# Kernel optimization log

Hardware: AMD Instinct MI355X
Metric: run time of the kernel (lower is better)

The kernel has to match this reference:

```python
import jax, jax.numpy as jnp
import numpy as np

B, S, H, D = 8, 4096, 16, 128

def setup_inputs() -> dict:
    key = jax.random.key(0)
    kq, kk, kv = jax.random.split(key, 3)
    q = jax.random.normal(kq, (B, S, H, D), dtype=jnp.float32)
    k = jax.random.normal(kk, (B, S, H, D), dtype=jnp.float32)
    v = jax.random.normal(kv, (B, S, H, D), dtype=jnp.float32)
    return {"q": q, "k": k, "v": v}

def reference(q, k, v):
    # Efficient (linear) attention: softmax K over sequence, softmax Q over feature dim,
    # then context = K^T V per (batch, head), out = Q @ context. Vectorized over heads.
    k_sm = jax.nn.softmax(k, axis=1)          # softmax over S  (B,S,H,D)
    q_sm = jax.nn.softmax(q, axis=-1)         # softmax over D  (B,S,H,D)
    context = jnp.einsum('bshd,bshe->bhde', k_sm, v)   # (B,H,Dk,Dv)
    out = jnp.einsum('bshd,bhde->bshe', q_sm, context) # (B,S,H,Dv)
    return out
```

## Files before the change

kernel.cpp:

```cpp
#include <hip/hip_runtime.h>

using bf16x8 = __attribute__((ext_vector_type(8))) short;
using f32x4  = __attribute__((ext_vector_type(4))) float;

static constexpr int NB = 8;
static constexpr int NS = 4096;
static constexpr int NH = 16;
static constexpr int ND = 128;
static constexpr int BH = NB * NH;
static constexpr int HD = NH * ND;

__device__ inline unsigned pack2(float a, float b) {
    unsigned ua = __float_as_uint(a), ub = __float_as_uint(b);
    ua += 0x7fffu + ((ua >> 16) & 1u);
    ub += 0x7fffu + ((ub >> 16) & 1u);
    return (ua >> 16) | (ub & 0xffff0000u);
}

__device__ inline int swzh(int row) { return (row ^ (row >> 2)) & 7; }

template <int NC>
__global__ __launch_bounds__(256, 2)
void ctx_mfma(const float* __restrict__ kk, const float* __restrict__ vv,
              float* __restrict__ pctx_t, float* __restrict__ pden) {
    constexpr int SC = NS / NC;
    constexpr int T  = SC / 64;
    __shared__ __align__(16) unsigned short aL[2][128][64];
    __shared__ __align__(16) unsigned short bL[2][128][64];

    const int blk = blockIdx.x, bh = blk / NC, c = blk % NC;
    const int b = bh >> 4, h = bh & 15;
    const int tid = threadIdx.x, lane = tid & 63, wv = tid >> 6;
    const int r15 = lane & 15, hi = lane >> 4;
    const size_t base = (size_t)b * NS * HD + (size_t)h * ND;

    const int d0 = (tid & 31) * 4;
    const int sg = tid >> 5;

    float dsum[4] = {0.f, 0.f, 0.f, 0.f};

    auto stage = [&](int t, int buf) {
        const size_t s0 = (size_t)(c * SC + t * 64 + 8 * sg);
        const float* kp = kk + base + s0 * HD + d0;
        const float* vp = vv + base + s0 * HD + d0;
        float4 kq[8], vq[8];
#pragma unroll
        for (int j = 0; j < 8; ++j) kq[j] = *(const float4*)(kp + (size_t)j * HD);
#pragma unroll
        for (int j = 0; j < 8; ++j) vq[j] = *(const float4*)(vp + (size_t)j * HD);
        float ek[8][4];
        const float* kf = (const float*)kq;
        const float* vf = (const float*)vq;
#pragma unroll
        for (int j = 0; j < 8; ++j)
#pragma unroll
            for (int i = 0; i < 4; ++i) {
                ek[j][i] = __expf(kf[4 * j + i]);
                dsum[i] += ek[j][i];
            }
#pragma unroll
        for (int i = 0; i < 4; ++i) {
            const int row = d0 + i;
            const int cw = sg ^ swzh(row);
            *(uint4*)&aL[buf][row][cw * 8] = make_uint4(
                pack2(ek[0][i], ek[1][i]), pack2(ek[2][i], ek[3][i]),
                pack2(ek[4][i], ek[5][i]), pack2(ek[6][i], ek[7][i]));
            *(uint4*)&bL[buf][row][cw * 8] = make_uint4(
                pack2(vf[0 + i], vf[4 + i]), pack2(vf[8 + i], vf[12 + i]),
                pack2(vf[16 + i], vf[20 + i]), pack2(vf[24 + i], vf[28 + i]));
        }
    };

    f32x4 acc[4][4];
#pragma unroll
    for (int m = 0; m < 4; ++m)
#pragma unroll
        for (int n = 0; n < 4; ++n) acc[m][n] = (f32x4){0.f, 0.f, 0.f, 0.f};

    const int wd = wv >> 1, we = wv & 1;

    stage(0, 0);
    for (int t = 0; t < T; ++t) {
        __syncthreads();
        if (t + 1 < T) stage(t + 1, (t + 1) & 1);
        const int buf = t & 1;
#pragma unroll
        for (int ks = 0; ks < 2; ++ks) {
            bf16x8 af[4], bfv[4];
#pragma unroll
            for (int m = 0; m < 4; ++m) {
                const int row = 64 * wd + 16 * m + r15;
                const int cw = (4 * ks + hi) ^ swzh(row);
                af[m] = *(const bf16x8*)&aL[buf][row][cw * 8];
            }
#pragma unroll
            for (int n = 0; n < 4; ++n) {
                const int row = 64 * we + 16 * n + r15;
                const int cw = (4 * ks + hi) ^ swzh(row);
                bfv[n] = *(const bf16x8*)&bL[buf][row][cw * 8];
            }
#pragma unroll
            for (int m = 0; m < 4; ++m)
#pragma unroll
                for (int n = 0; n < 4; ++n)
                    acc[m][n] = __builtin_amdgcn_mfma_f32_16x16x32_bf16(
                        af[m], bfv[n], acc[m][n], 0, 0, 0);
        }
    }

    __syncthreads();
    float* dr = (float*)&aL[0][0][0];
    *(float4*)&dr[sg * 128 + d0] = make_float4(dsum[0], dsum[1], dsum[2], dsum[3]);
    __syncthreads();
    if (tid < 128) {
        float s = 0.f;
#pragma unroll
        for (int r = 0; r < 8; ++r) s += dr[r * 128 + tid];
        pden[(size_t)blk * 128 + tid] = s;
    }

    float* po = pctx_t + (size_t)blk * (ND * ND);
#pragma unroll
    for (int m = 0; m < 4; ++m)
#pragma unroll
        for (int n = 0; n < 4; ++n) {
            const int e  = 64 * we + 16 * n + r15;
            const int dd = 64 * wd + 16 * m + 4 * hi;
            *(f32x4*)&po[e * ND + dd] = acc[m][n];
        }
}

__global__ void ctx_combine(const float* __restrict__ pctx_t,
                            const float* __restrict__ pden,
                            unsigned short* __restrict__ ctx_t, int nc) {
    const int gid = blockIdx.x * 256 + threadIdx.x;
    const size_t w = (size_t)gid * 2;
    const int bh = (int)(w >> 14);
    const int wi = (int)(w & 16383);
    const int dd = wi & 127;
    float s0 = 0.f, s1 = 0.f, dn0 = 0.f, dn1 = 0.f;
    for (int c2 = 0; c2 < nc; ++c2) {
        const float* p  = pctx_t + (((size_t)(bh * nc + c2)) << 14) + wi;
        const float* pd = pden + (size_t)(bh * nc + c2) * ND + dd;
        s0 += p[0]; s1 += p[1];
        dn0 += pd[0]; dn1 += pd[1];
    }
    *(unsigned*)&ctx_t[w] = pack2(s0 / dn0, s1 / dn1);
}

__global__ __launch_bounds__(256, 2)
void out_mfma(const float* __restrict__ qq,
              const unsigned short* __restrict__ ctx_t,
              float* __restrict__ out) {
    __shared__ __align__(16) unsigned short cL[128][128];
    __shared__ __align__(16) unsigned short qL[2][32][128];
    __shared__ float qd[2][32];

    const int blk = blockIdx.x, bh = blk >> 3, c = blk & 7;
    const int b = bh >> 4, h = bh & 15;
    const int tid = threadIdx.x, lane = tid & 63, wv = tid >> 6;
    const int r15 = lane & 15, hi = lane >> 4;

    {
        const unsigned short* src = ctx_t + ((size_t)bh << 14);
#pragma unroll
        for (int j = 0; j < 8; ++j) {
            const int g = tid + 256 * j;
            const int e = g >> 4, cs = g & 15;
            uint4 t4 = *(const uint4*)&src[e * 128 + cs * 8];
            *(uint4*)&cL[e][(cs ^ (e & 15)) * 8] = t4;
        }
    }

    const size_t qbase = (size_t)b * NS * HD + (size_t)h * ND;
    const int s_blk = c * 512;

    auto stageq = [&](int t, int buf) {
#pragma unroll
        for (int jj = 0; jj < 2; ++jj) {
            const int g = tid + 256 * jj;
            const int s = g >> 4, cs = g & 15;
            const float* qp = qq + qbase + (size_t)(s_blk + t * 32 + s) * HD + cs * 8;
            float x[8];
            *(float4*)&x[0] = *(const float4*)qp;
            *(float4*)&x[4] = *(const float4*)(qp + 4);
            float ps = 0.f;
            unsigned pw[4];
#pragma unroll
            for (int j2 = 0; j2 < 4; ++j2) {
                float e0 = __expf(x[2 * j2]), e1 = __expf(x[2 * j2 + 1]);
                ps += e0 + e1;
                pw[j2] = pack2(e0, e1);
            }
            ps += __shfl_xor(ps, 1);
            ps += __shfl_xor(ps, 2);
            ps += __shfl_xor(ps, 4);
            ps += __shfl_xor(ps, 8);
            *(uint4*)&qL[buf][s][(cs ^ (s & 15)) * 8] =
                make_uint4(pw[0], pw[1], pw[2], pw[3]);
            if ((lane & 15) == 0) qd[buf][s] = ps;
        }
    };

    __syncthreads();

    bf16x8 bfr[2][4];
#pragma unroll
    for (int n = 0; n < 2; ++n) {
        const int e = 32 * wv + 16 * n + r15;
#pragma unroll
        for (int ks = 0; ks < 4; ++ks) {
            const int cw = (4 * ks + hi) ^ (e & 15);
            bfr[n][ks] = *(const bf16x8*)&cL[e][cw * 8];
        }
    }

    stageq(0, 0);
    for (int t = 0; t < 16; ++t) {
        __syncthreads();
        if (t + 1 < 16) stageq(t + 1, (t + 1) & 1);
        const int buf = t & 1;

        f32x4 acc[2][2];
#pragma unroll
        for (int m = 0; m < 2; ++m)
#pragma unroll
            for (int n = 0; n < 2; ++n) acc[m][n] = (f32x4){0.f, 0.f, 0.f, 0.f};

#pragma unroll
        for (int ks = 0; ks < 4; ++ks) {
            bf16x8 af[2];
#pragma unroll
            for (int m = 0; m < 2; ++m) {
                const int s = 16 * m + r15;
                const int cw = (4 * ks + hi) ^ (s & 15);
                af[m] = *(const bf16x8*)&qL[buf][s][cw * 8];
            }
#pragma unroll
            for (int m = 0; m < 2; ++m)
#pragma unroll
                for (int n = 0; n < 2; ++n)
                    acc[m][n] = __builtin_amdgcn_mfma_f32_16x16x32_bf16(
                        af[m], bfr[n][ks], acc[m][n], 0, 0, 0);
        }

#pragma unroll
        for (int m = 0; m < 2; ++m) {
            const int sl0 = 16 * m + 4 * hi;
            const float i0 = 1.f / qd[buf][sl0];
            const float i1 = 1.f / qd[buf][sl0 + 1];
            const float i2 = 1.f / qd[buf][sl0 + 2];
            const float i3 = 1.f / qd[buf][sl0 + 3];
            const int srow = s_blk + t * 32 + sl0;
            float* ob = out + ((size_t)b * NS + srow) * HD + (size_t)h * ND;
#pragma unroll
            for (int n = 0; n < 2; ++n) {
                const int e = 32 * wv + 16 * n + r15;
                ob[0 * HD + e] = acc[m][n][0] * i0;
                ob[1 * HD + e] = acc[m][n][1] * i1;
                ob[2 * HD + e] = acc[m][n][2] * i2;
                ob[3 * HD + e] = acc[m][n][3] * i3;
            }
        }
    }
}

extern "C" void kernel_launch(void* const* d_in, const int* in_sizes, int n_in,
                              void* d_out, int out_size, void* d_ws, size_t ws_size,
                              hipStream_t stream) {
    (void)in_sizes; (void)n_in; (void)out_size;
    const float* q = (const float*)d_in[0];
    const float* k = (const float*)d_in[1];
    const float* v = (const float*)d_in[2];
    float* out = (float*)d_out;

    auto need = [](size_t nc) -> size_t {
        return 4ull * ((size_t)BH * nc * ND * ND + (size_t)BH * nc * ND) +
               2ull * (size_t)BH * ND * ND;
    };
    const int nc = (ws_size >= need(4)) ? 4 : (ws_size >= need(2)) ? 2 : 1;

    float* pctx_t = (float*)d_ws;
    float* pden   = pctx_t + (size_t)BH * nc * ND * ND;
    unsigned short* ctx_t = (unsigned short*)(pden + (size_t)BH * nc * ND);

    if (nc == 4)
        ctx_mfma<4><<<BH * 4, 256, 0, stream>>>(k, v, pctx_t, pden);
    else if (nc == 2)
        ctx_mfma<2><<<BH * 2, 256, 0, stream>>>(k, v, pctx_t, pden);
    else
        ctx_mfma<1><<<BH * 1, 256, 0, stream>>>(k, v, pctx_t, pden);

    ctx_combine<<<(BH * ND * ND / 2) / 256, 256, 0, stream>>>(pctx_t, pden, ctx_t, nc);

    out_mfma<<<BH * 8, 256, 0, stream>>>(q, ctx_t, out);
}
```

Baseline: 266.2 us.

## Register-prefetch K/V tiles with single LDS buffer and split sequence eight ways

Replaces the LDS double buffer with register double-buffering: global loads for the next tile are issued before the current tile is exponentiated, packed and stored to one shared LDS buffer, with two barriers per tile. LDS use is halved and launch bounds go up to 3 blocks per CU to raise occupancy. The host also picks an 8-way sequence split when the workspace allows, launching more blocks but adding partial-context traffic for the combine kernel. Risks include extra barriers, register pressure from holding two tiles in registers, and whether the workspace is large enough for the 8-way path.

```diff
diff --git a/kernel.cpp b/kernel.cpp
--- a/kernel.cpp
+++ b/kernel.cpp
@@ -19,14 +19,35 @@
 
 __device__ inline int swzh(int row) { return (row ^ (row >> 2)) & 7; }
 
+__device__ inline void pack_tile(const float4* kq, const float4* vq,
+                                 float dsum[4], uint4 pa[4], uint4 pb[4]) {
+    const float* kf = (const float*)kq;
+    const float* vf = (const float*)vq;
+#pragma unroll
+    for (int i = 0; i < 4; ++i) {
+        float e[8];
+#pragma unroll
+        for (int j = 0; j < 8; ++j) {
+            e[j] = __expf(kf[4 * j + i]);
+            dsum[i] += e[j];
+        }
+        pa[i] = make_uint4(pack2(e[0], e[1]), pack2(e[2], e[3]),
+                           pack2(e[4], e[5]), pack2(e[6], e[7]));
+        pb[i] = make_uint4(pack2(vf[0 + i], vf[4 + i]),
+                           pack2(vf[8 + i], vf[12 + i]),
+                           pack2(vf[16 + i], vf[20 + i]),
+                           pack2(vf[24 + i], vf[28 + i]));
+    }
+}
+
 template <int NC>
-__global__ __launch_bounds__(256, 2)
+__global__ __launch_bounds__(256, 3)
 void ctx_mfma(const float* __restrict__ kk, const float* __restrict__ vv,
               float* __restrict__ pctx_t, float* __restrict__ pden) {
     constexpr int SC = NS / NC;
     constexpr int T  = SC / 64;
-    __shared__ __align__(16) unsigned short aL[2][128][64];
-    __shared__ __align__(16) unsigned short bL[2][128][64];
+    __shared__ __align__(16) unsigned short aL[128][64];
+    __shared__ __align__(16) unsigned short bL[128][64];
 
     const int blk = blockIdx.x, bh = blk / NC, c = blk % NC;
     const int b = bh >> 4, h = bh & 15;
@@ -39,35 +60,23 @@
 
     float dsum[4] = {0.f, 0.f, 0.f, 0.f};
 
-    auto stage = [&](int t, int buf) {
+    auto issue = [&](int t, float4* kq, float4* vq) {
         const size_t s0 = (size_t)(c * SC + t * 64 + 8 * sg);
         const float* kp = kk + base + s0 * HD + d0;
         const float* vp = vv + base + s0 * HD + d0;
-        float4 kq[8], vq[8];
 #pragma unroll
         for (int j = 0; j < 8; ++j) kq[j] = *(const float4*)(kp + (size_t)j * HD);
 #pragma unroll
         for (int j = 0; j < 8; ++j) vq[j] = *(const float4*)(vp + (size_t)j * HD);
-        float ek[8][4];
-        const float* kf = (const float*)kq;
-        const float* vf = (const float*)vq;
-#pragma unroll
-        for (int j = 0; j < 8; ++j)
-#pragma unroll
-            for (int i = 0; i < 4; ++i) {
-                ek[j][i] = __expf(kf[4 * j + i]);
-                dsum[i] += ek[j][i];
-            }
+    };
+
+    auto store_tile = [&](const uint4* pa, const uint4* pb) {
 #pragma unroll
         for (int i = 0; i < 4; ++i) {
             const int row = d0 + i;
             const int cw = sg ^ swzh(row);
-            *(uint4*)&aL[buf][row][cw * 8] = make_uint4(
-                pack2(ek[0][i], ek[1][i]), pack2(ek[2][i], ek[3][i]),
-                pack2(ek[4][i], ek[5][i]), pack2(ek[6][i], ek[7][i]));
-            *(uint4*)&bL[buf][row][cw * 8] = make_uint4(
-                pack2(vf[0 + i], vf[4 + i]), pack2(vf[8 + i], vf[12 + i]),
-                pack2(vf[16 + i], vf[20 + i]), pack2(vf[24 + i], vf[28 + i]));
+            *(uint4*)&aL[row][cw * 8] = pa[i];
+            *(uint4*)&bL[row][cw * 8] = pb[i];
         }
     };
 
@@ -79,11 +88,7 @@
 
     const int wd = wv >> 1, we = wv & 1;
 
-    stage(0, 0);
-    for (int t = 0; t < T; ++t) {
-        __syncthreads();
-        if (t + 1 < T) stage(t + 1, (t + 1) & 1);
-        const int buf = t & 1;
+    auto mma = [&]() {
 #pragma unroll
         for (int ks = 0; ks < 2; ++ks) {
             bf16x8 af[4], bfv[4];
@@ -91,13 +96,13 @@
             for (int m = 0; m < 4; ++m) {
                 const int row = 64 * wd + 16 * m + r15;
                 const int cw = (4 * ks + hi) ^ swzh(row);
-                af[m] = *(const bf16x8*)&aL[buf][row][cw * 8];
+                af[m] = *(const bf16x8*)&aL[row][cw * 8];
             }
 #pragma unroll
             for (int n = 0; n < 4; ++n) {
                 const int row = 64 * we + 16 * n + r15;
                 const int cw = (4 * ks + hi) ^ swzh(row);
-                bfv[n] = *(const bf16x8*)&bL[buf][row][cw * 8];
+                bfv[n] = *(const bf16x8*)&bL[row][cw * 8];
             }
 #pragma unroll
             for (int m = 0; m < 4; ++m)
@@ -106,10 +111,34 @@
                     acc[m][n] = __builtin_amdgcn_mfma_f32_16x16x32_bf16(
                         af[m], bfv[n], acc[m][n], 0, 0, 0);
         }
+    };
+
+    float4 ka[8], va[8], kb[8], vb[8];
+    issue(0, ka, va);
+
+    for (int t = 0; t < T; t += 2) {
+        if (t + 1 < T) issue(t + 1, kb, vb);
+        {
+            uint4 pa[4], pb[4];
+            pack_tile(ka, va, dsum, pa, pb);
+            __syncthreads();
+            store_tile(pa, pb);
+            __syncthreads();
+            mma();
+        }
+        if (t + 2 < T) issue(t + 2, ka, va);
+        {
+            uint4 pa[4], pb[4];
+            pack_tile(kb, vb, dsum, pa, pb);
+            __syncthreads();
+            store_tile(pa, pb);
+            __syncthreads();
+            mma();
+        }
     }
 
     __syncthreads();
-    float* dr = (float*)&aL[0][0][0];
+    float* dr = (float*)&aL[0][0];
     *(float4*)&dr[sg * 128 + d0] = make_float4(dsum[0], dsum[1], dsum[2], dsum[3]);
     __syncthreads();
     if (tid < 128) {
@@ -278,13 +307,17 @@
         return 4ull * ((size_t)BH * nc * ND * ND + (size_t)BH * nc * ND) +
                2ull * (size_t)BH * ND * ND;
     };
-    const int nc = (ws_size >= need(4)) ? 4 : (ws_size >= need(2)) ? 2 : 1;
+    const int nc = (ws_size >= need(8)) ? 8
+                 : (ws_size >= need(4)) ? 4
+                 : (ws_size >= need(2)) ? 2 : 1;
 
     float* pctx_t = (float*)d_ws;
     float* pden   = pctx_t + (size_t)BH * nc * ND * ND;
     unsigned short* ctx_t = (unsigned short*)(pden + (size_t)BH * nc * ND);
 
-    if (nc == 4)
+    if (nc == 8)
+        ctx_mfma<8><<<BH * 8, 256, 0, stream>>>(k, v, pctx_t, pden);
+    else if (nc == 4)
         ctx_mfma<4><<<BH * 4, 256, 0, stream>>>(k, v, pctx_t, pden);
     else if (nc == 2)
         ctx_mfma<2><<<BH * 2, 256, 0, stream>>>(k, v, pctx_t, pden);
```

After: 561.3 us. 111% more time.

## Prefetch next K/V tile into registers while MFMA consumes current LDS tile

Applied to the files above, without the earlier changes.

Restructures the main loop into a register-level software pipeline. Each iteration now packs the tile already held in registers, issues global loads for the next tile, writes the packed data to LDS, syncs, and runs the MFMAs. The aim is to overlap global-load latency with the exp/pack work and the matrix multiply, instead of loading and waiting inside the same stage. In exchange it keeps 16 float4 values live across the MFMA section, which adds register pressure under launch_bounds(256,2).

```diff
diff --git a/kernel.cpp b/kernel.cpp
--- a/kernel.cpp
+++ b/kernel.cpp
@@ -18,6 +18,27 @@
 }
 
 __device__ inline int swzh(int row) { return (row ^ (row >> 2)) & 7; }
+
+__device__ inline void pack_tile(const float4* kq, const float4* vq,
+                                 float dsum[4], uint4 pa[4], uint4 pb[4]) {
+    const float* kf = (const float*)kq;
+    const float* vf = (const float*)vq;
+#pragma unroll
+    for (int i = 0; i < 4; ++i) {
+        float e[8];
+#pragma unroll
+        for (int j = 0; j < 8; ++j) {
+            e[j] = __expf(kf[4 * j + i]);
+            dsum[i] += e[j];
+        }
+        pa[i] = make_uint4(pack2(e[0], e[1]), pack2(e[2], e[3]),
+                           pack2(e[4], e[5]), pack2(e[6], e[7]));
+        pb[i] = make_uint4(pack2(vf[0 + i], vf[4 + i]),
+                           pack2(vf[8 + i], vf[12 + i]),
+                           pack2(vf[16 + i], vf[20 + i]),
+                           pack2(vf[24 + i], vf[28 + i]));
+    }
+}
 
 template <int NC>
 __global__ __launch_bounds__(256, 2)
@@ -39,35 +60,23 @@
 
     float dsum[4] = {0.f, 0.f, 0.f, 0.f};
 
-    auto stage = [&](int t, int buf) {
+    auto issue = [&](int t, float4* kq, float4* vq) {
         const size_t s0 = (size_t)(c * SC + t * 64 + 8 * sg);
         const float* kp = kk + base + s0 * HD + d0;
         const float* vp = vv + base + s0 * HD + d0;
-        float4 kq[8], vq[8];
 #pragma unroll
         for (int j = 0; j < 8; ++j) kq[j] = *(const float4*)(kp + (size_t)j * HD);
 #pragma unroll
         for (int j = 0; j < 8; ++j) vq[j] = *(const float4*)(vp + (size_t)j * HD);
-        float ek[8][4];
-        const float* kf = (const float*)kq;
-        const float* vf = (const float*)vq;
-#pragma unroll
-        for (int j = 0; j < 8; ++j)
-#pragma unroll
-            for (int i = 0; i < 4; ++i) {
-                ek[j][i] = __expf(kf[4 * j + i]);
-                dsum[i] += ek[j][i];
-            }
+    };
+
+    auto store_tile = [&](int buf, const uint4* pa, const uint4* pb) {
 #pragma unroll
         for (int i = 0; i < 4; ++i) {
             const int row = d0 + i;
             const int cw = sg ^ swzh(row);
-            *(uint4*)&aL[buf][row][cw * 8] = make_uint4(
-                pack2(ek[0][i], ek[1][i]), pack2(ek[2][i], ek[3][i]),
-                pack2(ek[4][i], ek[5][i]), pack2(ek[6][i], ek[7][i]));
-            *(uint4*)&bL[buf][row][cw * 8] = make_uint4(
-                pack2(vf[0 + i], vf[4 + i]), pack2(vf[8 + i], vf[12 + i]),
-                pack2(vf[16 + i], vf[20 + i]), pack2(vf[24 + i], vf[28 + i]));
+            *(uint4*)&aL[buf][row][cw * 8] = pa[i];
+            *(uint4*)&bL[buf][row][cw * 8] = pb[i];
         }
     };
 
@@ -79,11 +88,7 @@
 
     const int wd = wv >> 1, we = wv & 1;
 
-    stage(0, 0);
-    for (int t = 0; t < T; ++t) {
-        __syncthreads();
-        if (t + 1 < T) stage(t + 1, (t + 1) & 1);
-        const int buf = t & 1;
+    auto mma = [&](int buf) {
 #pragma unroll
         for (int ks = 0; ks < 2; ++ks) {
             bf16x8 af[4], bfv[4];
@@ -106,6 +111,18 @@
                     acc[m][n] = __builtin_amdgcn_mfma_f32_16x16x32_bf16(
                         af[m], bfv[n], acc[m][n], 0, 0, 0);
         }
+    };
+
+    float4 kq[8], vq[8];
+    issue(0, kq, vq);
+
+    for (int t = 0; t < T; ++t) {
+        uint4 pa[4], pb[4];
+        pack_tile(kq, vq, dsum, pa, pb);
+        if (t + 1 < T) issue(t + 1, kq, vq);
+        store_tile(t & 1, pa, pb);
+        __syncthreads();
+        mma(t & 1);
     }
 
     __syncthreads();
```

Result: no change. 263.1 us (-1.1%).

## Shrink ctx tile to 32 rows, register-prefetch next tile, allow 8-way split

Applied to the files above, without the earlier changes.

The K^T V context kernel now stages 32 sequence rows per iteration instead of 64 and halves its LDS buffers. It issues global loads for the next tile into registers before writing the current tile to shared memory, and raises the occupancy hint from 2 to 3 blocks per CU. The host can also pick an 8-way sequence split when the workspace is large enough, which launches more blocks. The aim is better latency hiding and more parallelism, paid for with more barriers per element, a larger partial buffer for the combine step, and a new swizzle that must stay bank-conflict free.

```diff
diff --git a/kernel.cpp b/kernel.cpp
--- a/kernel.cpp
+++ b/kernel.cpp
@@ -17,16 +17,16 @@
     return (ua >> 16) | (ub & 0xffff0000u);
 }
 
-__device__ inline int swzh(int row) { return (row ^ (row >> 2)) & 7; }
+__device__ inline int swz2(int row) { return (row ^ (row >> 2)) & 3; }
 
 template <int NC>
-__global__ __launch_bounds__(256, 2)
+__global__ __launch_bounds__(256, 3)
 void ctx_mfma(const float* __restrict__ kk, const float* __restrict__ vv,
               float* __restrict__ pctx_t, float* __restrict__ pden) {
     constexpr int SC = NS / NC;
-    constexpr int T  = SC / 64;
-    __shared__ __align__(16) unsigned short aL[2][128][64];
-    __shared__ __align__(16) unsigned short bL[2][128][64];
+    constexpr int T  = SC / 32;
+    __shared__ __align__(16) unsigned short aL[2][128][32];
+    __shared__ __align__(16) unsigned short bL[2][128][32];
 
     const int blk = blockIdx.x, bh = blk / NC, c = blk % NC;
     const int b = bh >> 4, h = bh & 15;
@@ -39,73 +39,73 @@
 
     float dsum[4] = {0.f, 0.f, 0.f, 0.f};
 
-    auto stage = [&](int t, int buf) {
-        const size_t s0 = (size_t)(c * SC + t * 64 + 8 * sg);
+    auto issue = [&](int t, float4* kq, float4* vq) {
+        const size_t s0 = (size_t)(c * SC + t * 32 + 4 * sg);
         const float* kp = kk + base + s0 * HD + d0;
         const float* vp = vv + base + s0 * HD + d0;
-        float4 kq[8], vq[8];
-#pragma unroll
-        for (int j = 0; j < 8; ++j) kq[j] = *(const float4*)(kp + (size_t)j * HD);
-#pragma unroll
-        for (int j = 0; j < 8; ++j) vq[j] = *(const float4*)(vp + (size_t)j * HD);
-        float ek[8][4];
+#pragma unroll
+        for (int j = 0; j < 4; ++j) kq[j] = *(const float4*)(kp + (size_t)j * HD);
+#pragma unroll
+        for (int j = 0; j < 4; ++j) vq[j] = *(const float4*)(vp + (size_t)j * HD);
+    };
+
+    f32x4 acc[4][4];
+#pragma unroll
+    for (int m = 0; m < 4; ++m)
+#pragma unroll
+        for (int n = 0; n < 4; ++n) acc[m][n] = (f32x4){0.f, 0.f, 0.f, 0.f};
+
+    const int wd = wv >> 1, we = wv & 1;
+
+    auto mma = [&](int buf) {
+        bf16x8 af[4], bfv[4];
+#pragma unroll
+        for (int m = 0; m < 4; ++m) {
+            const int row = 64 * wd + 16 * m + r15;
+            const int pc0 = (2 * hi) ^ (swz2(row) << 1);
+            af[m] = *(const bf16x8*)&aL[buf][row][pc0 * 4];
+        }
+#pragma unroll
+        for (int n = 0; n < 4; ++n) {
+            const int row = 64 * we + 16 * n + r15;
+            const int pc0 = (2 * hi) ^ (swz2(row) << 1);
+            bfv[n] = *(const bf16x8*)&bL[buf][row][pc0 * 4];
+        }
+#pragma unroll
+        for (int m = 0; m < 4; ++m)
+#pragma unroll
+            for (int n = 0; n < 4; ++n)
+                acc[m][n] = __builtin_amdgcn_mfma_f32_16x16x32_bf16(
+                    af[m], bfv[n], acc[m][n], 0, 0, 0);
+    };
+
+    float4 kq[4], vq[4];
+    issue(0, kq, vq);
+
+    for (int t = 0; t < T; ++t) {
         const float* kf = (const float*)kq;
         const float* vf = (const float*)vq;
-#pragma unroll
-        for (int j = 0; j < 8; ++j)
-#pragma unroll
-            for (int i = 0; i < 4; ++i) {
-                ek[j][i] = __expf(kf[4 * j + i]);
-                dsum[i] += ek[j][i];
-            }
+        uint2 pa[4], pb[4];
+#pragma unroll
+        for (int i = 0; i < 4; ++i) {
+            float e0 = __expf(kf[0 + i]), e1 = __expf(kf[4 + i]);
+            float e2 = __expf(kf[8 + i]), e3 = __expf(kf[12 + i]);
+            dsum[i] += (e0 + e1) + (e2 + e3);
+            pa[i] = make_uint2(pack2(e0, e1), pack2(e2, e3));
+            pb[i] = make_uint2(pack2(vf[0 + i], vf[4 + i]),
+                               pack2(vf[8 + i], vf[12 + i]));
+        }
+        if (t + 1 < T) issue(t + 1, kq, vq);
+        const int buf = t & 1;
 #pragma unroll
         for (int i = 0; i < 4; ++i) {
             const int row = d0 + i;
-            const int cw = sg ^ swzh(row);
-            *(uint4*)&aL[buf][row][cw * 8] = make_uint4(
-                pack2(ek[0][i], ek[1][i]), pack2(ek[2][i], ek[3][i]),
-                pack2(ek[4][i], ek[5][i]), pack2(ek[6][i], ek[7][i]));
-            *(uint4*)&bL[buf][row][cw * 8] = make_uint4(
-                pack2(vf[0 + i], vf[4 + i]), pack2(vf[8 + i], vf[12 + i]),
-                pack2(vf[16 + i], vf[20 + i]), pack2(vf[24 + i], vf[28 + i]));
-        }
-    };
-
-    f32x4 acc[4][4];
-#pragma unroll
-    for (int m = 0; m < 4; ++m)
-#pragma unroll
-        for (int n = 0; n < 4; ++n) acc[m][n] = (f32x4){0.f, 0.f, 0.f, 0.f};
-
-    const int wd = wv >> 1, we = wv & 1;
-
-    stage(0, 0);
-    for (int t = 0; t < T; ++t) {
+            const int slot = sg ^ (swz2(row) << 1);
+            *(uint2*)&aL[buf][row][slot * 4] = pa[i];
+            *(uint2*)&bL[buf][row][slot * 4] = pb[i];
+        }
         __syncthreads();
-        if (t + 1 < T) stage(t + 1, (t + 1) & 1);
-        const int buf = t & 1;
-#pragma unroll
-        for (int ks = 0; ks < 2; ++ks) {
-            bf16x8 af[4], bfv[4];
-#pragma unroll
-            for (int m = 0; m < 4; ++m) {
-                const int row = 64 * wd + 16 * m + r15;
-                const int cw = (4 * ks + hi) ^ swzh(row);
-                af[m] = *(const bf16x8*)&aL[buf][row][cw * 8];
-            }
-#pragma unroll
-            for (int n = 0; n < 4; ++n) {
-                const int row = 64 * we + 16 * n + r15;
-                const int cw = (4 * ks + hi) ^ swzh(row);
-                bfv[n] = *(const bf16x8*)&bL[buf][row][cw * 8];
-            }
-#pragma unroll
-            for (int m = 0; m < 4; ++m)
-#pragma unroll
-                for (int n = 0; n < 4; ++n)
-                    acc[m][n] = __builtin_amdgcn_mfma_f32_16x16x32_bf16(
-                        af[m], bfv[n], acc[m][n], 0, 0, 0);
-        }
+        mma(buf);
     }
 
     __syncthreads();
@@ -278,13 +278,17 @@
         return 4ull * ((size_t)BH * nc * ND * ND + (size_t)BH * nc * ND) +
                2ull * (size_t)BH * ND * ND;
     };
-    const int nc = (ws_size >= need(4)) ? 4 : (ws_size >= need(2)) ? 2 : 1;
+    const int nc = (ws_size >= need(8)) ? 8
+                 : (ws_size >= need(4)) ? 4
+                 : (ws_size >= need(2)) ? 2 : 1;
 
     float* pctx_t = (float*)d_ws;
     float* pden   = pctx_t + (size_t)BH * nc * ND * ND;
     unsigned short* ctx_t = (unsigned short*)(pden + (size_t)BH * nc * ND);
 
-    if (nc == 4)
+    if (nc == 8)
+        ctx_mfma<8><<<BH * 8, 256, 0, stream>>>(k, v, pctx_t, pden);
+    else if (nc == 4)
         ctx_mfma<4><<<BH * 4, 256, 0, stream>>>(k, v, pctx_t, pden);
     else if (nc == 2)
         ctx_mfma<2><<<BH * 2, 256, 0, stream>>>(k, v, pctx_t, pden);
```

Result: no change. 265.9 us (-0.1%).
